# Optimization experiments

Measured on AMD Instinct MI355X. Metric: run time of the kernel, lower is better.

Reference implementation:

```python
import jax, jax.numpy as jnp
import numpy as np

B, S, D = 8, 1024, 768
H, DK = 12, 64
DFF = 3072
EPS = 1e-5


def setup_inputs() -> dict:
    key = jax.random.key(0)
    ks = jax.random.split(key, 12)
    s = lambda fan_in: 1.0 / np.sqrt(fan_in)
    return {
        "x": jax.random.normal(ks[0], (B, S, D), jnp.float32),
        "Wq": jax.random.normal(ks[1], (D, D), jnp.float32) * s(D),
        "Wk": jax.random.normal(ks[2], (D, D), jnp.float32) * s(D),
        "Wv": jax.random.normal(ks[3], (D, D), jnp.float32) * s(D),
        "Wo": jax.random.normal(ks[4], (D, D), jnp.float32) * s(D),
        "g1": jnp.ones((D,), jnp.float32),
        "b1": jnp.zeros((D,), jnp.float32),
        "g2": jnp.ones((D,), jnp.float32),
        "b2": jnp.zeros((D,), jnp.float32),
        "W1": jax.random.normal(ks[5], (D, DFF), jnp.float32) * s(D),
        "bW1": jnp.zeros((DFF,), jnp.float32),
        "W2": jax.random.normal(ks[6], (DFF, D), jnp.float32) * s(DFF),
        "bW2": jnp.zeros((D,), jnp.float32),
    }


def _layernorm(x, g, b):
    mu = x.mean(-1, keepdims=True)
    var = ((x - mu) ** 2).mean(-1, keepdims=True)
    return (x - mu) * jax.lax.rsqrt(var + EPS) * g + b


def reference(x, Wq, Wk, Wv, Wo, g1, b1, g2, b2, W1, bW1, W2, bW2):
    scale = DK ** (-0.5)
    # pre-norm attention block
    h = _layernorm(x, g1, b1)
    q = (h @ Wq).reshape(B, S, H, DK)
    k = (h @ Wk).reshape(B, S, H, DK)
    v = (h @ Wv).reshape(B, S, H, DK)
    logits = jnp.einsum("bqhd,bkhd->bhqk", q, k) * scale  # [B,H,S,S]
    weights = jax.nn.softmax(logits, axis=-1)
    attn = jnp.einsum("bhqk,bkhd->bqhd", weights, v).reshape(B, S, D)
    x = x + attn @ Wo
    # pre-norm FFN block
    h = _layernorm(x, g2, b2)
    h = jax.nn.gelu(h @ W1 + bW1, approximate=False)
    x = x + h @ W2 + bW2
    return x
```

## Files before the change

### kernel.cpp

```cpp
#include <hip/hip_runtime.h>
#include <cstdint>
#include <cstddef>

#define B_   8
#define S_   1024
#define D_   768
#define H_   12
#define DK_  64
#define DFF_ 3072
#define M_   (B_*S_)

typedef __attribute__((ext_vector_type(8))) short  short8;
typedef __attribute__((ext_vector_type(4))) short  short4v;
typedef __attribute__((ext_vector_type(8))) __bf16 bf16x8;
typedef __attribute__((ext_vector_type(4))) float  f32x4;
typedef __attribute__((ext_vector_type(4))) unsigned uint4v;
typedef __attribute__((ext_vector_type(2))) unsigned uint2v;

__device__ __forceinline__ unsigned short f2bf(float f) {
    unsigned u = __builtin_bit_cast(unsigned, f);
    u += 0x7FFFu + ((u >> 16) & 1u);
    return (unsigned short)(u >> 16);
}

__device__ __forceinline__ unsigned pkbf(float a, float b) {
    unsigned short ua = __builtin_bit_cast(unsigned short, (__bf16)a);
    unsigned short ub = __builtin_bit_cast(unsigned short, (__bf16)b);
    return (unsigned)ua | ((unsigned)ub << 16);
}

__device__ __forceinline__ f32x4 mfma16(short8 a, short8 b, f32x4 c) {
    return __builtin_amdgcn_mfma_f32_16x16x32_bf16(
        __builtin_bit_cast(bf16x8, a), __builtin_bit_cast(bf16x8, b), c, 0, 0, 0);
}

__device__ __forceinline__ void gload16(const void* g, void* l) {
    auto gp = reinterpret_cast<const __attribute__((address_space(1))) unsigned*>(
        reinterpret_cast<uintptr_t>(g));
    auto lp = reinterpret_cast<__attribute__((address_space(3))) unsigned*>(
        reinterpret_cast<uintptr_t>(l));
    __builtin_amdgcn_global_load_lds(gp, lp, 16, 0, 0);
}

__device__ __forceinline__ float gelu_f(float v) {
    return 0.5f * v * (1.0f + erff(v * 0.70710678118654752f));
}

__global__ __launch_bounds__(256) void wtrans4_kernel(
    const float* __restrict__ W0, const float* __restrict__ W1,
    const float* __restrict__ W2, const float* __restrict__ W3,
    unsigned short* __restrict__ Wt)
{
    __shared__ float tile[32][33];
    int z = blockIdx.z;
    const float* W = (z == 0) ? W0 : (z == 1) ? W1 : (z == 2) ? W2 : W3;
    unsigned short* dst = Wt + (size_t)z * 768 * 768;
    int n0 = blockIdx.x * 32, k0 = blockIdx.y * 32;
    int tx = threadIdx.x, ty = threadIdx.y;
#pragma unroll
    for (int j = 0; j < 4; ++j)
        tile[ty + j*8][tx] = W[(size_t)(k0 + ty + j*8) * 768 + n0 + tx];
    __syncthreads();
#pragma unroll
    for (int j = 0; j < 4; ++j)
        dst[(size_t)(n0 + ty + j*8) * 768 + k0 + tx] = f2bf(tile[tx][ty + j*8]);
}

__global__ __launch_bounds__(256) void wtrans_kernel(
    const float* __restrict__ W, unsigned short* __restrict__ Wt, int K, int N)
{
    __shared__ float tile[32][33];
    int n0 = blockIdx.x * 32, k0 = blockIdx.y * 32;
    int tx = threadIdx.x, ty = threadIdx.y;
#pragma unroll
    for (int j = 0; j < 4; ++j)
        tile[ty + j*8][tx] = W[(size_t)(k0 + ty + j*8) * N + n0 + tx];
    __syncthreads();
#pragma unroll
    for (int j = 0; j < 4; ++j)
        Wt[(size_t)(n0 + ty + j*8) * K + k0 + tx] = f2bf(tile[tx][ty + j*8]);
}

__global__ __launch_bounds__(256) void ln_kernel(
    const float* __restrict__ x, const float* __restrict__ g,
    const float* __restrict__ b, unsigned short* __restrict__ out)
{
    int row = blockIdx.x, t = threadIdx.x;
    const float* xr = x + (size_t)row * D_;
    float v[3];
#pragma unroll
    for (int i = 0; i < 3; ++i) v[i] = xr[t + i*256];
    float s  = v[0] + v[1] + v[2];
    float ss = v[0]*v[0] + v[1]*v[1] + v[2]*v[2];
#pragma unroll
    for (int d = 1; d < 64; d <<= 1) { s += __shfl_xor(s, d); ss += __shfl_xor(ss, d); }
    __shared__ float red[8];
    int w = t >> 6, lane = t & 63;
    if (lane == 0) { red[w] = s; red[4 + w] = ss; }
    __syncthreads();
    s  = red[0] + red[1] + red[2] + red[3];
    ss = red[4] + red[5] + red[6] + red[7];
    float mu   = s * (1.0f / D_);
    float var  = ss * (1.0f / D_) - mu * mu;
    float rstd = rsqrtf(var + 1e-5f);
    unsigned short* orow = out + (size_t)row * D_;
#pragma unroll
    for (int i = 0; i < 3; ++i) {
        int c = t + i*256;
        orow[c] = f2bf((v[i] - mu) * rstd * g[c] + b[c]);
    }
}

template<int BN, int EPI>
__global__ __launch_bounds__(256, 2) void gemm_kernel(
    const unsigned short* __restrict__ A, const unsigned short* __restrict__ Wt,
    const float* __restrict__ bias, const float* __restrict__ resid,
    void* __restrict__ outp, int N, int K)
{
    __shared__ unsigned short Al[2][128*64];
    __shared__ unsigned short Bl[2][BN*64];
    constexpr int NJ = BN / 64;
    constexpr int ASH = 4, BSH = 2*NJ;
    const int nbn = N / BN;
    const int nwg = gridDim.x;
    const int p = blockIdx.x;
    const int bid = (p & 7) * (nwg >> 3) + (p >> 3);
    const int bm = bid / nbn, bn = bid % nbn;
    const int t = threadIdx.x;
    const int lane = t & 63, w = t >> 6;
    const int wm = w >> 1, wn = w & 1;
    const int lr = lane & 15, lh = lane >> 4;
    const char* aBase = (const char*)(A  + (size_t)(bm*128) * K);
    const char* bBase = (const char*)(Wt + (size_t)(bn*BN)  * K);

    uintptr_t aAdr[ASH], bAdr[BSH];
#pragma unroll
    for (int s = 0; s < ASH; ++s) {
        int d = s*4096 + t*16;
        int row = d >> 7;
        int ch  = ((d >> 4) & 7) ^ (row & 7);
        aAdr[s] = (uintptr_t)aBase + (size_t)row*(K*2) + ch*16;
    }
#pragma unroll
    for (int s = 0; s < BSH; ++s) {
        int d = s*4096 + t*16;
        int row = d >> 7;
        int ch  = ((d >> 4) & 7) ^ (row & 7);
        bAdr[s] = (uintptr_t)bBase + (size_t)row*(K*2) + ch*16;
    }

    f32x4 acc[4][2*NJ] = {};

    auto stage = [&](int kt, int buf) {
        const int k0b = kt << 7;
#pragma unroll
        for (int s = 0; s < ASH; ++s)
            gload16((const void*)(aAdr[s] + k0b), (char*)&Al[buf][0] + s*4096 + t*16);
#pragma unroll
        for (int s = 0; s < BSH; ++s)
            gload16((const void*)(bAdr[s] + k0b), (char*)&Bl[buf][0] + s*4096 + t*16);
    };

    const int nk = K >> 6;
    stage(0, 0);
    stage(1, 1);

    for (int it = 0; it < nk; ++it) {
        const int buf = it & 1;
        if (it + 1 < nk) {
            if constexpr (BN == 128) asm volatile("s_waitcnt vmcnt(8)" ::: "memory");
            else                     asm volatile("s_waitcnt vmcnt(6)" ::: "memory");
        } else {
            asm volatile("s_waitcnt vmcnt(0)" ::: "memory");
        }
        __builtin_amdgcn_s_barrier();

        short8 af[2][4], bf[2][2*NJ];
#pragma unroll
        for (int kk = 0; kk < 2; ++kk) {
#pragma unroll
            for (int i = 0; i < 4; ++i)
                af[kk][i] = *reinterpret_cast<const short8*>(
                    &Al[buf][(wm*64 + i*16 + lr)*64 + (((kk*4 + lh) ^ (lr & 7))*8)]);
#pragma unroll
            for (int j = 0; j < 2*NJ; ++j)
                bf[kk][j] = *reinterpret_cast<const short8*>(
                    &Bl[buf][(wn*(32*NJ) + j*16 + lr)*64 + (((kk*4 + lh) ^ (lr & 7))*8)]);
        }
        __builtin_amdgcn_s_setprio(1);
#pragma unroll
        for (int kk = 0; kk < 2; ++kk)
#pragma unroll
            for (int i = 0; i < 4; ++i)
#pragma unroll
                for (int j = 0; j < 2*NJ; ++j)
                    acc[i][j] = mfma16(af[kk][i], bf[kk][j], acc[i][j]);
        __builtin_amdgcn_s_setprio(0);
        __builtin_amdgcn_s_barrier();
        if (it + 2 < nk) stage(it + 2, buf);
    }

#pragma unroll
    for (int i = 0; i < 4; ++i) {
#pragma unroll
        for (int r = 0; r < 4; ++r) {
            int row = bm*128 + wm*64 + i*16 + lh*4 + r;
#pragma unroll
            for (int j = 0; j < 2*NJ; ++j) {
                int col = bn*BN + wn*(32*NJ) + j*16 + lr;
                float v = acc[i][j][r];
                if (EPI == 0) {
                    ((unsigned short*)outp)[(size_t)row*N + col] = f2bf(v);
                } else if (EPI == 1) {
                    v += bias[col];
                    v = gelu_f(v);
                    ((unsigned short*)outp)[(size_t)row*N + col] = f2bf(v);
                } else {
                    if (bias) v += bias[col];
                    v += resid[(size_t)row*N + col];
                    ((float*)outp)[(size_t)row*N + col] = v;
                }
            }
        }
    }
}

template<int EPI>
__global__ __launch_bounds__(512, 2) void gemmb_kernel(
    const unsigned short* __restrict__ A, const unsigned short* __restrict__ Wt,
    const float* __restrict__ bias, const float* __restrict__ resid,
    void* __restrict__ outp, int N, int K)
{
    __shared__ unsigned short Al[2][256*64];
    __shared__ unsigned short Bl[2][128*64];
    const int nbn = N >> 7;
    const int nwg = gridDim.x;
    const int p = blockIdx.x;
    const int bid = (p & 7) * (nwg >> 3) + (p >> 3);
    const int bm = bid / nbn, bn = bid % nbn;
    const int t = threadIdx.x;
    const int lane = t & 63, w = t >> 6;
    const int wm = w >> 1, wn = w & 1;
    const int lr = lane & 15, lh = lane >> 4;
    const char* aBase = (const char*)(A  + (size_t)(bm*256) * K);
    const char* bBase = (const char*)(Wt + (size_t)(bn*128) * K);

    uintptr_t aAdr[4], bAdr[2];
#pragma unroll
    for (int s = 0; s < 4; ++s) {
        int d = s*8192 + t*16;
        int row = d >> 7;
        int ch  = ((d >> 4) & 7) ^ (row & 7);
        aAdr[s] = (uintptr_t)aBase + (size_t)row*(K*2) + ch*16;
    }
#pragma unroll
    for (int s = 0; s < 2; ++s) {
        int d = s*8192 + t*16;
        int row = d >> 7;
        int ch  = ((d >> 4) & 7) ^ (row & 7);
        bAdr[s] = (uintptr_t)bBase + (size_t)row*(K*2) + ch*16;
    }

    f32x4 acc[4][4] = {};

    auto stage = [&](int kt, int buf) {
        const int k0b = kt << 7;
#pragma unroll
        for (int s = 0; s < 4; ++s)
            gload16((const void*)(aAdr[s] + k0b), (char*)&Al[buf][0] + s*8192 + t*16);
#pragma unroll
        for (int s = 0; s < 2; ++s)
            gload16((const void*)(bAdr[s] + k0b), (char*)&Bl[buf][0] + s*8192 + t*16);
    };

    const int nk = K >> 6;
    stage(0, 0);
    stage(1, 1);

    for (int it = 0; it < nk; ++it) {
        const int buf = it & 1;
        if (it + 1 < nk) asm volatile("s_waitcnt vmcnt(6)" ::: "memory");
        else             asm volatile("s_waitcnt vmcnt(0)" ::: "memory");
        __builtin_amdgcn_s_barrier();

        short8 af[2][4], bf[2][4];
#pragma unroll
        for (int kk = 0; kk < 2; ++kk) {
#pragma unroll
            for (int i = 0; i < 4; ++i)
                af[kk][i] = *reinterpret_cast<const short8*>(
                    &Al[buf][(wm*64 + i*16 + lr)*64 + (((kk*4 + lh) ^ (lr & 7))*8)]);
#pragma unroll
            for (int j = 0; j < 4; ++j)
                bf[kk][j] = *reinterpret_cast<const short8*>(
                    &Bl[buf][(wn*64 + j*16 + lr)*64 + (((kk*4 + lh) ^ (lr & 7))*8)]);
        }
        __builtin_amdgcn_s_setprio(1);
#pragma unroll
        for (int kk = 0; kk < 2; ++kk)
#pragma unroll
            for (int i = 0; i < 4; ++i)
#pragma unroll
                for (int j = 0; j < 4; ++j)
                    acc[i][j] = mfma16(af[kk][i], bf[kk][j], acc[i][j]);
        __builtin_amdgcn_s_setprio(0);
        __builtin_amdgcn_s_barrier();
        if (it + 2 < nk) stage(it + 2, buf);
    }

#pragma unroll
    for (int i = 0; i < 4; ++i) {
#pragma unroll
        for (int r = 0; r < 4; ++r) {
            int row = bm*256 + wm*64 + i*16 + lh*4 + r;
#pragma unroll
            for (int j = 0; j < 4; ++j) {
                int col = bn*128 + wn*64 + j*16 + lr;
                float v = acc[i][j][r];
                if (EPI == 0) {
                    ((unsigned short*)outp)[(size_t)row*N + col] = f2bf(v);
                } else if (EPI == 1) {
                    v += bias[col];
                    v = gelu_f(v);
                    ((unsigned short*)outp)[(size_t)row*N + col] = f2bf(v);
                } else {
                    if (bias) v += bias[col];
                    v += resid[(size_t)row*N + col];
                    ((float*)outp)[(size_t)row*N + col] = v;
                }
            }
        }
    }
}

__global__ __launch_bounds__(256) void vtrans_kernel(
    const unsigned short* __restrict__ qkv, unsigned short* __restrict__ vt)
{
    __shared__ unsigned short tl[64][65];
    int bid = blockIdx.x;
    int sblk = bid & 15, bh = bid >> 4;
    int b = bh / H_, h = bh % H_;
    int t = threadIdx.x, tx = t & 63, ty = t >> 6;
    int s0 = sblk * 64;
#pragma unroll
    for (int j = 0; j < 16; ++j) {
        int s = j*4 + ty;
        tl[s][tx] = qkv[(size_t)(b*S_ + s0 + s)*2304 + 1536 + h*64 + tx];
    }
    __syncthreads();
#pragma unroll
    for (int j = 0; j < 16; ++j) {
        int dk = j*4 + ty;
        vt[((size_t)bh*64 + dk)*S_ + s0 + tx] = tl[tx][dk];
    }
}

__global__ __launch_bounds__(256, 3) void attn_kernel(
    const unsigned short* __restrict__ qkv, const unsigned short* __restrict__ vt,
    unsigned short* __restrict__ out)
{
    __shared__ unsigned short Kl[2][64*64];
    __shared__ unsigned short Vl[2][64*64];

    const int p = blockIdx.x;
    const int l = (p & 7) * 96 + (p >> 3);
    const int qb = l & 7, bh = l >> 3;
    const int b = bh / H_, h = bh % H_;
    const int t = threadIdx.x, lane = t & 63, w = t >> 6;
    const int lr = lane & 15, lh = lane >> 4;
    const int sz = (lr & 7) << 3;

    const float SC = 0.125f * 1.44269504089f;

    const int qrow0 = qb*128 + w*32;
    short8 bq[2][2];
#pragma unroll
    for (int qi = 0; qi < 2; ++qi) {
        const unsigned short* qp = qkv + (size_t)(b*S_ + qrow0 + qi*16 + lr)*2304 + h*64;
#pragma unroll
        for (int c = 0; c < 2; ++c)
            bq[qi][c] = *reinterpret_cast<const short8*>(&qp[c*32 + lh*8]);
    }

    float m_run[2] = {-1e30f, -1e30f};
    float l_run[2] = {0.f, 0.f};
    f32x4 o[2][4] = {};

    const char* kgbase = (const char*)qkv;
    const char* vgbase = (const char*)vt;

    auto stage = [&](int kb, int buf) {
        const int ks = kb * 64;
#pragma unroll
        for (int shot = 0; shot < 2; ++shot) {
            int d = shot*4096 + t*16;
            int row = d >> 7;
            int colb = d & 127;
            int sc = colb ^ ((row & 7) << 4);
            const char* ksrc = kgbase + ((size_t)(b*S_ + ks + row)*2304 + 768 + h*64)*2 + sc;
            gload16(ksrc, (char*)&Kl[buf][0] + d);
            const char* vsrc = vgbase + ((size_t)(bh*64 + row)*1024 + ks)*2 + sc;
            gload16(vsrc, (char*)&Vl[buf][0] + d);
        }
    };

    stage(0, 0);
    asm volatile("s_waitcnt vmcnt(0)" ::: "memory");
    __builtin_amdgcn_s_barrier();

    for (int kb = 0; kb < 16; ++kb) {
        const int buf = kb & 1;
        if (kb < 15) stage(kb + 1, buf ^ 1);

        short8 ak[4][2];
#pragma unroll
        for (int j = 0; j < 4; ++j)
#pragma unroll
            for (int c = 0; c < 2; ++c)
                ak[j][c] = *reinterpret_cast<const short8*>(
                    &Kl[buf][(j*16 + lr)*64 + ((c*32 + lh*8) ^ sz)]);

        short8 av[4][2];
#pragma unroll
        for (int j = 0; j < 4; ++j) {
            const unsigned short* vrow = &Vl[buf][(j*16 + lr)*64];
#pragma unroll
            for (int ks = 0; ks < 2; ++ks) {
                short4v lo = *reinterpret_cast<const short4v*>(&vrow[(ks*32 + lh*4)      ^ sz]);
                short4v hi = *reinterpret_cast<const short4v*>(&vrow[(ks*32 + 16 + lh*4) ^ sz]);
                av[j][ks] = __builtin_shufflevector(lo, hi, 0,1,2,3,4,5,6,7);
            }
        }

#pragma unroll
        for (int qi = 0; qi < 2; ++qi) {
            f32x4 s[4];
            __builtin_amdgcn_s_setprio(1);
#pragma unroll
            for (int j = 0; j < 4; ++j) {
                f32x4 z = {0.f, 0.f, 0.f, 0.f};
                z = mfma16(ak[j][0], bq[qi][0], z);
                z = mfma16(ak[j][1], bq[qi][1], z);
                s[j] = z;
            }
            __builtin_amdgcn_s_setprio(0);

            float m01 = fmaxf(fmaxf(s[0][0], s[0][1]), fmaxf(s[0][2], s[0][3]));
            float m1  = fmaxf(fmaxf(s[1][0], s[1][1]), fmaxf(s[1][2], s[1][3]));
            float m2  = fmaxf(fmaxf(s[2][0], s[2][1]), fmaxf(s[2][2], s[2][3]));
            float m3  = fmaxf(fmaxf(s[3][0], s[3][1]), fmaxf(s[3][2], s[3][3]));
            float mt = fmaxf(fmaxf(m01, m1), fmaxf(m2, m3)) * SC;
            mt = fmaxf(mt, __shfl_xor(mt, 16));
            mt = fmaxf(mt, __shfl_xor(mt, 32));

            if (__any(mt > m_run[qi] + 8.0f)) {
                float mn = fmaxf(m_run[qi], mt);
                float a  = exp2f(m_run[qi] - mn);
                m_run[qi] = mn;
                l_run[qi] *= a;
#pragma unroll
                for (int j = 0; j < 4; ++j)
#pragma unroll
                    for (int r = 0; r < 4; ++r) o[qi][j][r] *= a;
            }

            const float negm = -m_run[qi];
            float rs = 0.f;
#pragma unroll
            for (int j = 0; j < 4; ++j)
#pragma unroll
                for (int r = 0; r < 4; ++r) {
                    float pv = exp2f(__builtin_fmaf(s[j][r], SC, negm));
                    s[j][r] = pv;
                    rs += pv;
                }
            l_run[qi] += rs;

            uint4v u0 = { pkbf(s[0][0], s[0][1]), pkbf(s[0][2], s[0][3]),
                          pkbf(s[1][0], s[1][1]), pkbf(s[1][2], s[1][3]) };
            uint4v u1 = { pkbf(s[2][0], s[2][1]), pkbf(s[2][2], s[2][3]),
                          pkbf(s[3][0], s[3][1]), pkbf(s[3][2], s[3][3]) };
            short8 pb0 = __builtin_bit_cast(short8, u0);
            short8 pb1 = __builtin_bit_cast(short8, u1);

            __builtin_amdgcn_s_setprio(1);
#pragma unroll
            for (int j = 0; j < 4; ++j) {
                o[qi][j] = mfma16(av[j][0], pb0, o[qi][j]);
                o[qi][j] = mfma16(av[j][1], pb1, o[qi][j]);
            }
            __builtin_amdgcn_s_setprio(0);
        }

        asm volatile("s_waitcnt vmcnt(0)" ::: "memory");
        __builtin_amdgcn_s_barrier();
    }

#pragma unroll
    for (int qi = 0; qi < 2; ++qi) {
        float ls = l_run[qi];
        ls += __shfl_xor(ls, 16);
        ls += __shfl_xor(ls, 32);
        float inv = 1.0f / ls;
        int q = qrow0 + qi*16 + lr;
        unsigned short* orow = out + (size_t)(b*S_ + q)*D_ + h*64;
#pragma unroll
        for (int j = 0; j < 4; ++j) {
            uint2v vv = { pkbf(o[qi][j][0]*inv, o[qi][j][1]*inv),
                          pkbf(o[qi][j][2]*inv, o[qi][j][3]*inv) };
            *reinterpret_cast<uint2v*>(&orow[j*16 + lh*4]) = vv;
        }
    }
}

extern "C" void kernel_launch(void* const* d_in, const int* in_sizes, int n_in,
                              void* d_out, int out_size, void* d_ws, size_t ws_size,
                              hipStream_t stream)
{
    (void)in_sizes; (void)n_in; (void)out_size; (void)ws_size;
    const float* x   = (const float*)d_in[0];
    const float* Wq  = (const float*)d_in[1];
    const float* Wk  = (const float*)d_in[2];
    const float* Wv  = (const float*)d_in[3];
    const float* Wo  = (const float*)d_in[4];
    const float* g1  = (const float*)d_in[5];
    const float* b1  = (const float*)d_in[6];
    const float* g2  = (const float*)d_in[7];
    const float* b2  = (const float*)d_in[8];
    const float* W1  = (const float*)d_in[9];
    const float* bW1 = (const float*)d_in[10];
    const float* W2  = (const float*)d_in[11];
    const float* bW2 = (const float*)d_in[12];
    float* out = (float*)d_out;

    char* ws = (char*)d_ws;
    unsigned short* wt_qkv = (unsigned short*)(ws);
    unsigned short* wt_o   = (unsigned short*)(ws + 3538944);
    unsigned short* wt_1   = (unsigned short*)(ws + 4718592);
    unsigned short* wt_2   = (unsigned short*)(ws + 9437184);
    unsigned short* slotA  = (unsigned short*)(ws + 14155776);
    unsigned short* qkv    = (unsigned short*)(ws + 26738688);
    unsigned short* vt     = (unsigned short*)(ws + 64487424);
    unsigned short* ffm    = qkv;

    dim3 tb(32, 8);
    wtrans4_kernel<<<dim3(24,24,4), tb, 0, stream>>>(Wq, Wk, Wv, Wo, wt_qkv);
    wtrans_kernel<<<dim3(96,24), tb, 0, stream>>>(W1, wt_1, 768, 3072);
    wtrans_kernel<<<dim3(24,96), tb, 0, stream>>>(W2, wt_2, 3072, 768);

    ln_kernel<<<M_, 256, 0, stream>>>(x, g1, b1, slotA);
    gemm_kernel<128,0><<<1152, 256, 0, stream>>>(slotA, wt_qkv, nullptr, nullptr, qkv, 2304, 768);
    vtrans_kernel<<<1536, 256, 0, stream>>>(qkv, vt);
    attn_kernel<<<768, 256, 0, stream>>>(qkv, vt, slotA);
    gemm_kernel<64,2><<<768, 256, 0, stream>>>(slotA, wt_o, nullptr, x, (void*)out, 768, 768);
    ln_kernel<<<M_, 256, 0, stream>>>(out, g2, b2, slotA);
    gemmb_kernel<1><<<768, 512, 0, stream>>>(slotA, wt_1, bW1, nullptr, ffm, 3072, 768);
    gemm_kernel<64,2><<<768, 256, 0, stream>>>(ffm, wt_2, bW2, out, (void*)out, 768, 3072);
}
```

Measured before the change: 310.3 us.

## Use 256x256-tile GEMM with half-K double buffering for QKV and FFN1

Adds a 512-thread GEMM kernel with a 256x256 output tile (8 waves as 2x4, each wave computing 128x64). The K-tile is split into two 32-wide halves in a double-buffered LDS layout with a new XOR swizzle, and the next tile's halves are issued right after each barrier. It replaces the 128-wide GEMM for QKV and the 256x128 kernel for FFN1, aiming to raise operand reuse and cut global and LDS traffic per FLOP. The trade-off is about 128KB of LDS per block, which likely allows only one block per CU, and much coarser grids (288 and 384 blocks) that can leave a sizable partial last wave.

```diff
diff --git a/kernel.cpp b/kernel.cpp
--- a/kernel.cpp
+++ b/kernel.cpp
@@ -108,6 +108,104 @@
     for (int i = 0; i < 3; ++i) {
         int c = t + i*256;
         orow[c] = f2bf((v[i] - mu) * rstd * g[c] + b[c]);
+    }
+}
+
+template<int EPI>
+__global__ __launch_bounds__(512, 2) void gemm256_kernel(
+    const unsigned short* __restrict__ A, const unsigned short* __restrict__ Wt,
+    const float* __restrict__ bias, const float* __restrict__ resid,
+    void* __restrict__ outp, int N, int K)
+{
+    __shared__ unsigned short L[2][2][2][8192];
+    const int nbn = N >> 8;
+    const int nwg = gridDim.x;
+    const int p = blockIdx.x;
+    const int bid = (p & 7) * (nwg >> 3) + (p >> 3);
+    const int bm = bid / nbn, bn = bid % nbn;
+    const int t = threadIdx.x;
+    const int lane = t & 63, w = t >> 6;
+    const int wm = w >> 2, wn = w & 3;
+    const int lr = lane & 15, lh = lane >> 4;
+    const int slotR = (lh ^ ((lr >> 1) & 3)) * 8;
+
+    const char* aBase = (const char*)(A  + (size_t)(bm*256) * K);
+    const char* bBase = (const char*)(Wt + (size_t)(bn*256) * K);
+
+    uintptr_t aAdr[2], bAdr[2];
+#pragma unroll
+    for (int s = 0; s < 2; ++s) {
+        int d = s*8192 + t*16;
+        int row = d >> 6;
+        int oct = ((d >> 4) & 3) ^ ((row >> 1) & 3);
+        aAdr[s] = (uintptr_t)aBase + (size_t)row*(K*2) + oct*16;
+        bAdr[s] = (uintptr_t)bBase + (size_t)row*(K*2) + oct*16;
+    }
+
+    f32x4 acc[8][4] = {};
+
+    auto stage_half = [&](int kt, int h, int buf) {
+        const int kb = kt*128 + h*64;
+#pragma unroll
+        for (int s = 0; s < 2; ++s) {
+            gload16((const void*)(aAdr[s] + kb), (char*)&L[buf][h][0][0] + s*8192 + t*16);
+            gload16((const void*)(bAdr[s] + kb), (char*)&L[buf][h][1][0] + s*8192 + t*16);
+        }
+    };
+
+    const int nk = K >> 6;
+    stage_half(0, 0, 0);
+    stage_half(0, 1, 0);
+
+    for (int tI = 0; tI < nk; ++tI) {
+        const int buf = tI & 1;
+#pragma unroll
+        for (int h = 0; h < 2; ++h) {
+            if (tI == nk - 1 && h == 1) asm volatile("s_waitcnt vmcnt(0)" ::: "memory");
+            else                        asm volatile("s_waitcnt vmcnt(4)" ::: "memory");
+            __builtin_amdgcn_s_barrier();
+            if (tI + 1 < nk) stage_half(tI + 1, h, buf ^ 1);
+            const unsigned short* la = &L[buf][h][0][0];
+            const unsigned short* lb = &L[buf][h][1][0];
+            short8 af[8], bf[4];
+#pragma unroll
+            for (int i = 0; i < 8; ++i)
+                af[i] = *reinterpret_cast<const short8*>(&la[(wm*128 + i*16 + lr)*32 + slotR]);
+#pragma unroll
+            for (int j = 0; j < 4; ++j)
+                bf[j] = *reinterpret_cast<const short8*>(&lb[(wn*64 + j*16 + lr)*32 + slotR]);
+            __builtin_amdgcn_s_setprio(1);
+#pragma unroll
+            for (int i = 0; i < 8; ++i)
+#pragma unroll
+                for (int j = 0; j < 4; ++j)
+                    acc[i][j] = mfma16(af[i], bf[j], acc[i][j]);
+            __builtin_amdgcn_s_setprio(0);
+        }
+    }
+
+#pragma unroll
+    for (int i = 0; i < 8; ++i) {
+#pragma unroll
+        for (int r = 0; r < 4; ++r) {
+            int row = bm*256 + wm*128 + i*16 + lh*4 + r;
+#pragma unroll
+            for (int j = 0; j < 4; ++j) {
+                int col = bn*256 + wn*64 + j*16 + lr;
+                float v = acc[i][j][r];
+                if (EPI == 0) {
+                    ((unsigned short*)outp)[(size_t)row*N + col] = f2bf(v);
+                } else if (EPI == 1) {
+                    v += bias[col];
+                    v = gelu_f(v);
+                    ((unsigned short*)outp)[(size_t)row*N + col] = f2bf(v);
+                } else {
+                    if (bias) v += bias[col];
+                    v += resid[(size_t)row*N + col];
+                    ((float*)outp)[(size_t)row*N + col] = v;
+                }
+            }
+        }
     }
 }
 
@@ -225,114 +323,6 @@
     }
 }
 
-template<int EPI>
-__global__ __launch_bounds__(512, 2) void gemmb_kernel(
-    const unsigned short* __restrict__ A, const unsigned short* __restrict__ Wt,
-    const float* __restrict__ bias, const float* __restrict__ resid,
-    void* __restrict__ outp, int N, int K)
-{
-    __shared__ unsigned short Al[2][256*64];
-    __shared__ unsigned short Bl[2][128*64];
-    const int nbn = N >> 7;
-    const int nwg = gridDim.x;
-    const int p = blockIdx.x;
-    const int bid = (p & 7) * (nwg >> 3) + (p >> 3);
-    const int bm = bid / nbn, bn = bid % nbn;
-    const int t = threadIdx.x;
-    const int lane = t & 63, w = t >> 6;
-    const int wm = w >> 1, wn = w & 1;
-    const int lr = lane & 15, lh = lane >> 4;
-    const char* aBase = (const char*)(A  + (size_t)(bm*256) * K);
-    const char* bBase = (const char*)(Wt + (size_t)(bn*128) * K);
-
-    uintptr_t aAdr[4], bAdr[2];
-#pragma unroll
-    for (int s = 0; s < 4; ++s) {
-        int d = s*8192 + t*16;
-        int row = d >> 7;
-        int ch  = ((d >> 4) & 7) ^ (row & 7);
-        aAdr[s] = (uintptr_t)aBase + (size_t)row*(K*2) + ch*16;
-    }
-#pragma unroll
-    for (int s = 0; s < 2; ++s) {
-        int d = s*8192 + t*16;
-        int row = d >> 7;
-        int ch  = ((d >> 4) & 7) ^ (row & 7);
-        bAdr[s] = (uintptr_t)bBase + (size_t)row*(K*2) + ch*16;
-    }
-
-    f32x4 acc[4][4] = {};
-
-    auto stage = [&](int kt, int buf) {
-        const int k0b = kt << 7;
-#pragma unroll
-        for (int s = 0; s < 4; ++s)
-            gload16((const void*)(aAdr[s] + k0b), (char*)&Al[buf][0] + s*8192 + t*16);
-#pragma unroll
-        for (int s = 0; s < 2; ++s)
-            gload16((const void*)(bAdr[s] + k0b), (char*)&Bl[buf][0] + s*8192 + t*16);
-    };
-
-    const int nk = K >> 6;
-    stage(0, 0);
-    stage(1, 1);
-
-    for (int it = 0; it < nk; ++it) {
-        const int buf = it & 1;
-        if (it + 1 < nk) asm volatile("s_waitcnt vmcnt(6)" ::: "memory");
-        else             asm volatile("s_waitcnt vmcnt(0)" ::: "memory");
-        __builtin_amdgcn_s_barrier();
-
-        short8 af[2][4], bf[2][4];
-#pragma unroll
-        for (int kk = 0; kk < 2; ++kk) {
-#pragma unroll
-            for (int i = 0; i < 4; ++i)
-                af[kk][i] = *reinterpret_cast<const short8*>(
-                    &Al[buf][(wm*64 + i*16 + lr)*64 + (((kk*4 + lh) ^ (lr & 7))*8)]);
-#pragma unroll
-            for (int j = 0; j < 4; ++j)
-                bf[kk][j] = *reinterpret_cast<const short8*>(
-                    &Bl[buf][(wn*64 + j*16 + lr)*64 + (((kk*4 + lh) ^ (lr & 7))*8)]);
-        }
-        __builtin_amdgcn_s_setprio(1);
-#pragma unroll
-        for (int kk = 0; kk < 2; ++kk)
-#pragma unroll
-            for (int i = 0; i < 4; ++i)
-#pragma unroll
-                for (int j = 0; j < 4; ++j)
-                    acc[i][j] = mfma16(af[kk][i], bf[kk][j], acc[i][j]);
-        __builtin_amdgcn_s_setprio(0);
-        __builtin_amdgcn_s_barrier();
-        if (it + 2 < nk) stage(it + 2, buf);
-    }
-
-#pragma unroll
-    for (int i = 0; i < 4; ++i) {
-#pragma unroll
-        for (int r = 0; r < 4; ++r) {
-            int row = bm*256 + wm*64 + i*16 + lh*4 + r;
-#pragma unroll
-            for (int j = 0; j < 4; ++j) {
-                int col = bn*128 + wn*64 + j*16 + lr;
-                float v = acc[i][j][r];
-                if (EPI == 0) {
-                    ((unsigned short*)outp)[(size_t)row*N + col] = f2bf(v);
-                } else if (EPI == 1) {
-                    v += bias[col];
-                    v = gelu_f(v);
-                    ((unsigned short*)outp)[(size_t)row*N + col] = f2bf(v);
-                } else {
-                    if (bias) v += bias[col];
-                    v += resid[(size_t)row*N + col];
-                    ((float*)outp)[(size_t)row*N + col] = v;
-                }
-            }
-        }
-    }
-}
-
 __global__ __launch_bounds__(256) void vtrans_kernel(
     const unsigned short* __restrict__ qkv, unsigned short* __restrict__ vt)
 {
@@ -549,11 +539,11 @@
     wtrans_kernel<<<dim3(24,96), tb, 0, stream>>>(W2, wt_2, 3072, 768);
 
     ln_kernel<<<M_, 256, 0, stream>>>(x, g1, b1, slotA);
-    gemm_kernel<128,0><<<1152, 256, 0, stream>>>(slotA, wt_qkv, nullptr, nullptr, qkv, 2304, 768);
+    gemm256_kernel<0><<<288, 512, 0, stream>>>(slotA, wt_qkv, nullptr, nullptr, qkv, 2304, 768);
     vtrans_kernel<<<1536, 256, 0, stream>>>(qkv, vt);
     attn_kernel<<<768, 256, 0, stream>>>(qkv, vt, slotA);
     gemm_kernel<64,2><<<768, 256, 0, stream>>>(slotA, wt_o, nullptr, x, (void*)out, 768, 768);
     ln_kernel<<<M_, 256, 0, stream>>>(out, g2, b2, slotA);
-    gemmb_kernel<1><<<768, 512, 0, stream>>>(slotA, wt_1, bW1, nullptr, ffm, 3072, 768);
+    gemm256_kernel<1><<<384, 512, 0, stream>>>(slotA, wt_1, bW1, nullptr, ffm, 3072, 768);
     gemm_kernel<64,2><<<768, 256, 0, stream>>>(ffm, wt_2, bW2, out, (void*)out, 768, 3072);
 }
```

Measured after the change: 314.6 us. About the same (+1.4%).
